# Performance work log

Measured on AMD Instinct MI355X. Metric: run time of the kernel, lower is better.

Reference implementation:

```python
import jax, jax.numpy as jnp
import numpy as np
import math

B, T, C = 8, 1024, 1024
H = 16
D = C // H
TI = 256
FF = 4 * C
EPS = 1e-5


def _ln(x, g, b):
    mu = jnp.mean(x, axis=-1, keepdims=True)
    var = jnp.mean(jnp.square(x - mu), axis=-1, keepdims=True)
    return (x - mu) * jax.lax.rsqrt(var + EPS) * g + b


def _gelu_tanh(x):
    return jax.nn.gelu(x, approximate=True)


def setup_inputs() -> dict:
    key = jax.random.key(0)
    ks = jax.random.split(key, 16)
    s = 0.02
    inp = {
        'x': jax.random.normal(ks[0], (B, T, C), jnp.float32),
        'x_img_feats': jax.random.normal(ks[1], (B, TI, C), jnp.float32),
        'ln1_g': jnp.ones((C,), jnp.float32), 'ln1_b': jnp.zeros((C,), jnp.float32),
        'ln2_g': jnp.ones((C,), jnp.float32), 'ln2_b': jnp.zeros((C,), jnp.float32),
        'W_attn': jax.random.normal(ks[2], (C, 3 * C), jnp.float32) * s,
        'b_attn': jnp.zeros((3 * C,), jnp.float32),
        'W_aproj': jax.random.normal(ks[3], (C, C), jnp.float32) * s,
        'b_aproj': jnp.zeros((C,), jnp.float32),
        'Wq': jax.random.normal(ks[4], (C, C), jnp.float32) * s,
        'bq': jnp.zeros((C,), jnp.float32),
        'Wk': jax.random.normal(ks[5], (C, C), jnp.float32) * s,
        'bk': jnp.zeros((C,), jnp.float32),
        'Wv': jax.random.normal(ks[6], (C, C), jnp.float32) * s,
        'bv': jnp.zeros((C,), jnp.float32),
        'Wcproj': jax.random.normal(ks[7], (C, C), jnp.float32) * s,
        'bcproj': jnp.zeros((C,), jnp.float32),
        'W_fc': jax.random.normal(ks[8], (C, FF), jnp.float32) * s,
        'b_fc': jnp.zeros((FF,), jnp.float32),
        'W_mproj': jax.random.normal(ks[9], (FF, C), jnp.float32) * s,
        'b_mproj': jnp.zeros((C,), jnp.float32),
    }
    return inp


def _heads(t):
    # (B, S, C) -> (B, H, S, D)
    return t.reshape(t.shape[0], t.shape[1], H, D).transpose(0, 2, 1, 3)


def _merge(t):
    # (B, H, S, D) -> (B, S, C)
    return t.transpose(0, 2, 1, 3).reshape(t.shape[0], t.shape[2], C)


def reference(x, x_img_feats, ln1_g, ln1_b, ln2_g, ln2_b,
              W_attn, b_attn, W_aproj, b_aproj,
              Wq, bq, Wk, bk, Wv, bv, Wcproj, bcproj,
              W_fc, b_fc, W_mproj, b_mproj):
    scale = 1.0 / math.sqrt(D)

    # causal self-attention
    h = _ln(x, ln1_g, ln1_b)
    qkv = h @ W_attn + b_attn
    q, k, v = jnp.split(qkv, 3, axis=-1)
    q, k, v = _heads(q), _heads(k), _heads(v)
    att = jnp.einsum('bhtd,bhsd->bhts', q, k) * scale
    causal = jnp.tril(jnp.ones((T, T), bool))
    att = jnp.where(causal[None, None], att, -jnp.inf)
    att = jax.nn.softmax(att, axis=-1)
    sa = _merge(jnp.einsum('bhts,bhsd->bhtd', att, v)) @ W_aproj + b_aproj
    x = x + sa

    # cross-attention (text queries, image keys/values)
    ht = _ln(x, ln1_g, ln1_b)
    q = _heads(ht @ Wq + bq)
    k = _heads(x_img_feats @ Wk + bk)
    v = _heads(x_img_feats @ Wv + bv)
    catt = jax.nn.softmax(jnp.einsum('bhtd,bhsd->bhts', q, k) * scale, axis=-1)
    ca = _merge(jnp.einsum('bhts,bhsd->bhtd', catt, v)) @ Wcproj + bcproj
    x = x + ca

    # MLP
    h2 = _ln(x, ln2_g, ln2_b)
    x = x + _gelu_tanh(h2 @ W_fc + b_fc) @ W_mproj + b_mproj
    return x
```

## Files before the change

### kernel.cpp

```cpp
#include <hip/hip_runtime.h>

#define B_ 8
#define T_ 1024
#define C_ 1024
#define H_ 16
#define D_ 64
#define TI_ 256
#define FF_ 4096
#define BT_ (B_*T_)
#define BTI_ (B_*TI_)

typedef __bf16 bf16x8 __attribute__((ext_vector_type(8)));
typedef float f32x4 __attribute__((ext_vector_type(4)));
typedef float f32x16 __attribute__((ext_vector_type(16)));

__device__ __forceinline__ unsigned short f2bf(float f){
  unsigned u = __float_as_uint(f);
  u += 0x7fffu + ((u>>16)&1u);
  return (unsigned short)(u>>16);
}

__device__ __forceinline__ void cp16(const void* g, void* l){
  __builtin_amdgcn_global_load_lds(
      (const __attribute__((address_space(1))) unsigned int*)(unsigned long long)g,
      (__attribute__((address_space(3))) unsigned int*)(unsigned long long)l,
      16, 0, 0);
}

template<int MODE>
__global__ __launch_bounds__(256, 3) void gemm_bt(
    const unsigned short* __restrict__ A,
    const unsigned short* __restrict__ Bt,
    const float* __restrict__ bias,
    const float* __restrict__ resid,
    void* __restrict__ outp,
    int M, int N, int K, int nkind, int tshift)
{
  __shared__ unsigned short sA[128*64];
  __shared__ unsigned short sB[128*64];
  const int tid  = threadIdx.x;
  const int wid  = tid >> 6;
  const int lane = tid & 63;
  const int l32  = lane & 31;
  const int khalf = lane >> 5;

  const int row0 = blockIdx.y * 128;
  const int col0 = blockIdx.x * 128;
  const int wr = (wid >> 1) * 64;
  const int wc = (wid & 1) * 64;

  const unsigned short* gp[8];
  unsigned short* lp[8];
#pragma unroll
  for (int r=0;r<8;r++){
    int chunk = wid*8 + r;
    int cA = chunk & 15;
    int slot = cA*64 + lane;
    int row = slot >> 3;
    int cc = (slot & 7) ^ (row & 7);
    if (chunk < 16){
      gp[r] = A  + (size_t)(row0+row)*K + cc*8;
      lp[r] = sA + cA*512;
    } else {
      gp[r] = Bt + (size_t)(col0+row)*K + cc*8;
      lp[r] = sB + cA*512;
    }
  }

  f32x16 acc[2][2];
#pragma unroll
  for (int i=0;i<2;i++)
#pragma unroll
    for (int j=0;j<2;j++)
#pragma unroll
      for (int r=0;r<16;r++) acc[i][j][r] = 0.f;

  for (int k0 = 0; k0 < K; k0 += 64){
    if (k0) __syncthreads();
#pragma unroll
    for (int r=0;r<8;r++)
      cp16(gp[r] + k0, lp[r]);
    __syncthreads();
    const char* sAb = (const char*)sA;
    const char* sBb = (const char*)sB;
#pragma unroll
    for (int kk=0;kk<4;kk++){
      bf16x8 af[2], bfb[2];
#pragma unroll
      for (int i=0;i<2;i++){
        int rr = wr + i*32 + l32;
        af[i] = *(const bf16x8*)(sAb + rr*128 + ((((kk<<1)+khalf) ^ (rr&7))<<4));
      }
#pragma unroll
      for (int j=0;j<2;j++){
        int rr = wc + j*32 + l32;
        bfb[j] = *(const bf16x8*)(sBb + rr*128 + ((((kk<<1)+khalf) ^ (rr&7))<<4));
      }
#pragma unroll
      for (int i=0;i<2;i++)
#pragma unroll
        for (int j=0;j<2;j++)
          acc[i][j] = __builtin_amdgcn_mfma_f32_32x32x16_bf16(af[i], bfb[j], acc[i][j], 0, 0, 0);
    }
  }

#pragma unroll
  for (int j=0;j<2;j++){
    int gc = col0 + wc + j*32 + l32;
    float bz = bias[gc];
#pragma unroll
    for (int i=0;i<2;i++){
      int gr_base = row0 + wr + i*32 + 4*khalf;
#pragma unroll
      for (int reg=0; reg<16; ++reg){
        int gr = gr_base + (reg&3) + 8*(reg>>2);
        float v = acc[i][j][reg] + bz;
        if (MODE == 1){
          float w = 1.5957691216057308f*(v + 0.044715f*v*v*v);
          float g = v / (1.f + __expf(-w));
          ((unsigned short*)outp)[(size_t)gr*N + gc] = f2bf(g);
        } else if (MODE == 2){
          size_t idx = (size_t)gr*N + gc;
          ((float*)outp)[idx] = resid[idx] + v;
        } else {
          int kind = gc >> 10;
          int hc = gc & 1023;
          int hh = hc >> 6;
          int d  = hc & 63;
          int bb = gr >> tshift;
          int tt = gr & ((1<<tshift)-1);
          size_t oidx = ((((size_t)(bb*16 + hh)*nkind + kind) << tshift) + tt)*64 + d;
          ((unsigned short*)outp)[oidx] = f2bf(v);
        }
      }
    }
  }
}

__global__ __launch_bounds__(256) void ln_fwd(
    const float* __restrict__ x, const float* __restrict__ g,
    const float* __restrict__ b, unsigned short* __restrict__ out)
{
  int row = blockIdx.x, t = threadIdx.x;
  const float4* xv = (const float4*)(x + (size_t)row*C_);
  float4 v = xv[t];
  float s  = v.x+v.y+v.z+v.w;
  float ss = v.x*v.x + v.y*v.y + v.z*v.z + v.w*v.w;
#pragma unroll
  for (int o=32;o>0;o>>=1){ s += __shfl_down(s,o); ss += __shfl_down(ss,o); }
  __shared__ float red[16];
  int wid = t>>6, lane = t&63;
  if (lane==0){ red[wid]=s; red[8+wid]=ss; }
  __syncthreads();
  if (t==0){
    red[0] = red[0]+red[1]+red[2]+red[3];
    red[8] = red[8]+red[9]+red[10]+red[11];
  }
  __syncthreads();
  float mu  = red[0] * (1.f/C_);
  float var = red[8] * (1.f/C_) - mu*mu;
  float rstd = rsqrtf(var + 1e-5f);
  float4 gv = ((const float4*)g)[t];
  float4 bv = ((const float4*)b)[t];
  ushort4 o;
  o.x = f2bf((v.x-mu)*rstd*gv.x + bv.x);
  o.y = f2bf((v.y-mu)*rstd*gv.y + bv.y);
  o.z = f2bf((v.z-mu)*rstd*gv.z + bv.z);
  o.w = f2bf((v.w-mu)*rstd*gv.w + bv.w);
  ((ushort4*)(out + (size_t)row*C_))[t] = o;
}

__global__ void wconv_t(const float* __restrict__ W, unsigned short* __restrict__ Wt,
                        int Kd, int Nd)
{
  __shared__ float tile[32][33];
  int tx = threadIdx.x, ty = threadIdx.y;
  int n0 = blockIdx.x*32, k0 = blockIdx.y*32;
#pragma unroll
  for (int j=0;j<4;j++)
    tile[ty+8*j][tx] = W[(size_t)(k0+ty+8*j)*Nd + (n0+tx)];
  __syncthreads();
#pragma unroll
  for (int j=0;j<4;j++)
    Wt[(size_t)(n0+ty+8*j)*Kd + (k0+tx)] = f2bf(tile[tx][ty+8*j]);
}

__global__ void wconv_t5(const float* W0, const float* W1, const float* W2,
                         const float* W3, const float* W4,
                         unsigned short* O0, unsigned short* O1, unsigned short* O2,
                         unsigned short* O3, unsigned short* O4)
{
  __shared__ float tile[32][33];
  const float* Ws[5] = {W0,W1,W2,W3,W4};
  unsigned short* Os[5] = {O0,O1,O2,O3,O4};
  const float* W = Ws[blockIdx.z];
  unsigned short* Wt = Os[blockIdx.z];
  int tx = threadIdx.x, ty = threadIdx.y;
  int n0 = blockIdx.x*32, k0 = blockIdx.y*32;
#pragma unroll
  for (int j=0;j<4;j++)
    tile[ty+8*j][tx] = W[(size_t)(k0+ty+8*j)*1024 + (n0+tx)];
  __syncthreads();
#pragma unroll
  for (int j=0;j<4;j++)
    Wt[(size_t)(n0+ty+8*j)*1024 + (k0+tx)] = f2bf(tile[tx][ty+8*j]);
}

#define PREP_N1 (BT_*C_/4)
#define PREP_N2 (BTI_*C_/4)
__global__ void prep_misc(const float* __restrict__ x, float* __restrict__ xcur,
                          const float* __restrict__ ximg, unsigned short* __restrict__ ximg_bf,
                          const float* __restrict__ bk, const float* __restrict__ bv,
                          float* __restrict__ bkv)
{
  int i = blockIdx.x*256 + threadIdx.x;
  if (i < PREP_N1){
    ((float4*)xcur)[i] = ((const float4*)x)[i];
  } else if (i < PREP_N1 + PREP_N2){
    int k = i - PREP_N1;
    float4 v = ((const float4*)ximg)[k];
    ushort4 o; o.x=f2bf(v.x); o.y=f2bf(v.y); o.z=f2bf(v.z); o.w=f2bf(v.w);
    ((ushort4*)ximg_bf)[k] = o;
  } else if (i < PREP_N1 + PREP_N2 + 512){
    int k = i - PREP_N1 - PREP_N2;
    ((float4*)bkv)[k] = (k < 256) ? ((const float4*)bk)[k] : ((const float4*)bv)[k-256];
  }
}

__global__ __launch_bounds__(256) void attn_fwd(
    const unsigned short* __restrict__ Qb, unsigned int sQ,
    const unsigned short* __restrict__ Kb, const unsigned short* __restrict__ Vb,
    unsigned int sKV, int causal, int nkb_in,
    unsigned short* __restrict__ Out, float scale)
{
  __shared__ unsigned short sK[64*64];
  __shared__ unsigned short sV[64*64];
  __shared__ unsigned short sP[4*16*64];
  const int tid = threadIdx.x;
  const int wid = tid >> 6;
  const int lane = tid & 63;
  const int quad = lane >> 4;
  const int l16 = lane & 15;

  const int L = blockIdx.x;
  const int g  = (L & 7) + (L >> 7) * 8;
  const int qt = 15 - ((L >> 3) & 15);
  const int b = g >> 4, h = g & 15;
  const float c2 = scale * 1.4426950408889634f;

  const unsigned short* Qp = Qb + (size_t)g * sQ;
  const unsigned short* Kp = Kb + (size_t)g * sKV;
  const unsigned short* Vp = Vb + (size_t)g * sKV;

  const int qrow = qt*64 + wid*16 + l16;
  const unsigned short* qb = Qp + (size_t)qrow*64;
  bf16x8 qf[2];
  qf[0] = *(const bf16x8*)(qb + quad*8);
  qf[1] = *(const bf16x8*)(qb + 32 + quad*8);

  f32x4 zero = {0.f,0.f,0.f,0.f};
  f32x4 O[4];
#pragma unroll
  for (int j=0;j<4;j++) O[j] = zero;
  float mrun[4], lrun[4];
#pragma unroll
  for (int r=0;r<4;r++){ mrun[r] = -1e30f; lrun[r] = 0.f; }

  const int nkb = causal ? (qt+1) : nkb_in;
  char* sPw = (char*)sP + wid*2048;

  for (int kb=0; kb<nkb; ++kb){
    if (kb) __syncthreads();
#pragma unroll
    for (int ss=0; ss<2; ++ss){
      int slot = tid + ss*256;
      int srow = slot >> 3;
      int cc = (slot & 7) ^ (srow & 7);
      cp16(Kp + (size_t)kb*4096 + srow*64 + cc*8, sK + (size_t)(wid*64 + ss*256)*8);
    }
    {
      int s_ = lane;
      int dbase = wid*16;
      const unsigned short* gv = Vp + (size_t)kb*4096 + s_*64 + dbase;
      unsigned short vals[16];
      *(uint4*)(vals)   = *(const uint4*)(gv);
      *(uint4*)(vals+8) = *(const uint4*)(gv+8);
      int chunk = s_ >> 3;
      int sb = (s_ & 7)*2;
#pragma unroll
      for (int jj=0; jj<16; ++jj){
        int d = dbase + jj;
        *(unsigned short*)((char*)sV + d*128 + ((chunk ^ (d&7))<<4) + sb) = vals[jj];
      }
    }
    __syncthreads();

    f32x4 sacc[4];
#pragma unroll
    for (int j=0;j<4;j++) sacc[j] = zero;
#pragma unroll
    for (int j=0;j<4;j++){
      int krow = j*16 + l16;
#pragma unroll
      for (int kk=0;kk<2;kk++){
        bf16x8 kf = *(const bf16x8*)((const char*)sK + krow*128 + (((kk*4+quad) ^ (krow&7))<<4));
        sacc[j] = __builtin_amdgcn_mfma_f32_16x16x32_bf16(qf[kk], kf, sacc[j], 0, 0, 0);
      }
    }
    const int qa0 = qt*64 + wid*16 + quad*4;
    float sc[4][4];
#pragma unroll
    for (int j=0;j<4;j++){
      int key = kb*64 + j*16 + l16;
#pragma unroll
      for (int r=0;r<4;r++){
        float v = sacc[j][r];
        if (causal && key > qa0 + r) v = -1e30f;
        sc[j][r] = v;
      }
    }
    float mnew[4], alpha[4], rs[4];
#pragma unroll
    for (int r=0;r<4;r++){
      float m = fmaxf(fmaxf(sc[0][r], sc[1][r]), fmaxf(sc[2][r], sc[3][r]));
#pragma unroll
      for (int msk=1; msk<16; msk<<=1) m = fmaxf(m, __shfl_xor(m, msk));
      mnew[r] = fmaxf(mrun[r], m);
      alpha[r] = exp2f((mrun[r] - mnew[r]) * c2);
      mrun[r] = mnew[r];
      rs[r] = 0.f;
    }
#pragma unroll
    for (int j=0;j<4;j++){
#pragma unroll
      for (int r=0;r<4;r++){
        float p = exp2f((sc[j][r] - mnew[r]) * c2);
        rs[r] += p;
        int prow = quad*4 + r;
        int cole = j*16 + l16;
        *(unsigned short*)(sPw + prow*128 + (((cole>>3) ^ (prow&7))<<4) + (cole&7)*2) = f2bf(p);
      }
    }
#pragma unroll
    for (int r=0;r<4;r++){
#pragma unroll
      for (int msk=1; msk<16; msk<<=1) rs[r] += __shfl_xor(rs[r], msk);
      lrun[r] = lrun[r]*alpha[r] + rs[r];
    }
#pragma unroll
    for (int j=0;j<4;j++){
      O[j][0] *= alpha[0]; O[j][1] *= alpha[1];
      O[j][2] *= alpha[2]; O[j][3] *= alpha[3];
    }
    bf16x8 pf[2];
#pragma unroll
    for (int kk=0;kk<2;kk++)
      pf[kk] = *(const bf16x8*)(sPw + l16*128 + (((kk*4+quad) ^ (l16&7))<<4));
#pragma unroll
    for (int j=0;j<4;j++){
      int vrow = j*16 + l16;
#pragma unroll
      for (int kk=0;kk<2;kk++){
        bf16x8 vf = *(const bf16x8*)((const char*)sV + vrow*128 + (((kk*4+quad) ^ (vrow&7))<<4));
        O[j] = __builtin_amdgcn_mfma_f32_16x16x32_bf16(pf[kk], vf, O[j], 0, 0, 0);
      }
    }
  }
#pragma unroll
  for (int j=0;j<4;j++){
#pragma unroll
    for (int r=0;r<4;r++){
      int qa = qt*64 + wid*16 + quad*4 + r;
      float o = O[j][r] / lrun[r];
      Out[(size_t)(b*T_ + qa)*C_ + h*64 + j*16 + l16] = f2bf(o);
    }
  }
}

extern "C" void kernel_launch(void* const* d_in, const int* in_sizes, int n_in,
                              void* d_out, int out_size, void* d_ws, size_t ws_size,
                              hipStream_t stream)
{
  const float* x       = (const float*)d_in[0];
  const float* ximg    = (const float*)d_in[1];
  const float* ln1_g   = (const float*)d_in[2];
  const float* ln1_b   = (const float*)d_in[3];
  const float* ln2_g   = (const float*)d_in[4];
  const float* ln2_b   = (const float*)d_in[5];
  const float* W_attn  = (const float*)d_in[6];
  const float* b_attn  = (const float*)d_in[7];
  const float* W_aproj = (const float*)d_in[8];
  const float* b_aproj = (const float*)d_in[9];
  const float* Wq = (const float*)d_in[10];
  const float* bq = (const float*)d_in[11];
  const float* Wk = (const float*)d_in[12];
  const float* bk = (const float*)d_in[13];
  const float* Wv = (const float*)d_in[14];
  const float* bv = (const float*)d_in[15];
  const float* Wcproj  = (const float*)d_in[16];
  const float* bcproj  = (const float*)d_in[17];
  const float* W_fc    = (const float*)d_in[18];
  const float* b_fc    = (const float*)d_in[19];
  const float* W_mproj = (const float*)d_in[20];
  const float* b_mproj = (const float*)d_in[21];

  char* ws = (char*)d_ws;
  unsigned short* wt_attn  = (unsigned short*)(ws + 0);
  unsigned short* wt_aproj = (unsigned short*)(ws + 6291456);
  unsigned short* wt_q     = (unsigned short*)(ws + 8388608);
  unsigned short* wt_k     = (unsigned short*)(ws + 10485760);
  unsigned short* wt_v     = (unsigned short*)(ws + 12582912);
  unsigned short* wt_cproj = (unsigned short*)(ws + 14680064);
  unsigned short* wt_fc    = (unsigned short*)(ws + 16777216);
  unsigned short* wt_mproj = (unsigned short*)(ws + 25165824);
  unsigned short* ximg_bf  = (unsigned short*)(ws + 33554432);
  float*          xcur     = (float*)(ws + 37748736);
  unsigned short* h_bf     = (unsigned short*)(ws + 71303168);
  unsigned short* qkv_hm   = (unsigned short*)(ws + 88080384);
  unsigned short* att_out  = (unsigned short*)(ws + 88080384 + 50331648);
  unsigned short* u_bf     = (unsigned short*)(ws + 88080384);
  unsigned short* q2_hm    = (unsigned short*)(ws + 155189248);
  unsigned short* kv2_hm   = (unsigned short*)(ws + 171966464);
  unsigned short* ca       = (unsigned short*)(ws + 180355072);
  float*          bkv      = (float*)(ws + 197132288);

  dim3 tb(32,8);
  wconv_t5<<<dim3(32,32,5), tb, 0, stream>>>(W_aproj, Wq, Wk, Wv, Wcproj,
                                             wt_aproj, wt_q, wt_k, wt_v, wt_cproj);
  wconv_t<<<dim3(96,32),  tb, 0, stream>>>(W_attn,  wt_attn,  1024, 3072);
  wconv_t<<<dim3(128,32), tb, 0, stream>>>(W_fc,    wt_fc,    1024, 4096);
  wconv_t<<<dim3(32,128), tb, 0, stream>>>(W_mproj, wt_mproj, 4096, 1024);
  prep_misc<<<(PREP_N1+PREP_N2+512+255)/256, 256, 0, stream>>>(
      x, xcur, ximg, ximg_bf, bk, bv, bkv);

  ln_fwd<<<BT_, 256, 0, stream>>>(x, ln1_g, ln1_b, h_bf);
  gemm_bt<3><<<dim3(24,64), 256, 0, stream>>>(h_bf, wt_attn, b_attn, nullptr, qkv_hm,
                                              BT_, 3072, 1024, 3, 10);
  attn_fwd<<<2048, 256, 0, stream>>>(qkv_hm, 3*T_*D_, qkv_hm + T_*D_, qkv_hm + 2*T_*D_,
                                     3*T_*D_, 1, 16, att_out, 0.125f);
  gemm_bt<2><<<dim3(8,64), 256, 0, stream>>>(att_out, wt_aproj, b_aproj, xcur, xcur,
                                             BT_, 1024, 1024, 0, 0);

  ln_fwd<<<BT_, 256, 0, stream>>>(xcur, ln1_g, ln1_b, h_bf);
  gemm_bt<3><<<dim3(8,64), 256, 0, stream>>>(h_bf, wt_q, bq, nullptr, q2_hm,
                                             BT_, 1024, 1024, 1, 10);
  gemm_bt<3><<<dim3(16,16), 256, 0, stream>>>(ximg_bf, wt_k, bkv, nullptr, kv2_hm,
                                              BTI_, 2048, 1024, 2, 8);
  attn_fwd<<<2048, 256, 0, stream>>>(q2_hm, T_*D_, kv2_hm, kv2_hm + TI_*D_,
                                     2*TI_*D_, 0, 4, ca, 0.125f);
  gemm_bt<2><<<dim3(8,64), 256, 0, stream>>>(ca, wt_cproj, bcproj, xcur, xcur,
                                             BT_, 1024, 1024, 0, 0);

  ln_fwd<<<BT_, 256, 0, stream>>>(xcur, ln2_g, ln2_b, h_bf);
  gemm_bt<1><<<dim3(32,64), 256, 0, stream>>>(h_bf, wt_fc, b_fc, nullptr, u_bf,
                                              BT_, 4096, 1024, 0, 0);
  gemm_bt<2><<<dim3(8,64), 256, 0, stream>>>(u_bf, wt_mproj, b_mproj, xcur, (float*)d_out,
                                             BT_, 1024, 4096, 0, 0);
}
```

Measured before the change: 722.2 us.

## Process two query tiles per attention block to reuse K/V loads

Each attention block now handles 128 query rows as two 64-row sub-tiles that share each K/V tile staged in LDS, which halves the grid size and the K/V global traffic per query. Causal masking is applied only on diagonal tiles, and fully masked sub-tiles are skipped. The softmax row sum now comes from an MFMA of P against a ones vector instead of shuffle reductions, and P is converted to bf16 by truncation rather than rounding. Costs: more registers per thread, fewer blocks to fill the GPU, and slightly different numerics in P and the row sum.

```diff
diff --git a/kernel.cpp b/kernel.cpp
--- a/kernel.cpp
+++ b/kernel.cpp
@@ -18,6 +18,9 @@
   unsigned u = __float_as_uint(f);
   u += 0x7fffu + ((u>>16)&1u);
   return (unsigned short)(u>>16);
+}
+__device__ __forceinline__ unsigned short f2bf_t(float f){
+  return (unsigned short)(__float_as_uint(f)>>16);
 }
 
 __device__ __forceinline__ void cp16(const void* g, void* l){
@@ -243,8 +246,9 @@
   const int l16 = lane & 15;
 
   const int L = blockIdx.x;
-  const int g  = (L & 7) + (L >> 7) * 8;
-  const int qt = 15 - ((L >> 3) & 15);
+  const int g  = (L & 7) + (L >> 6) * 8;
+  int qt = (L >> 3) & 7;
+  if (causal) qt = 7 - qt;
   const int b = g >> 4, h = g & 15;
   const float c2 = scale * 1.4426950408889634f;
 
@@ -252,21 +256,32 @@
   const unsigned short* Kp = Kb + (size_t)g * sKV;
   const unsigned short* Vp = Vb + (size_t)g * sKV;
 
-  const int qrow = qt*64 + wid*16 + l16;
-  const unsigned short* qb = Qp + (size_t)qrow*64;
-  bf16x8 qf[2];
-  qf[0] = *(const bf16x8*)(qb + quad*8);
-  qf[1] = *(const bf16x8*)(qb + 32 + quad*8);
+  bf16x8 qf[2][2];
+#pragma unroll
+  for (int s=0;s<2;s++){
+    int qrow = qt*128 + s*64 + wid*16 + l16;
+    const unsigned short* qb = Qp + (size_t)qrow*64;
+    qf[s][0] = *(const bf16x8*)(qb + quad*8);
+    qf[s][1] = *(const bf16x8*)(qb + 32 + quad*8);
+  }
+
+  bf16x8 ones;
+#pragma unroll
+  for (int k=0;k<8;k++) ones[k] = (__bf16)1.0f;
 
   f32x4 zero = {0.f,0.f,0.f,0.f};
-  f32x4 O[4];
-#pragma unroll
-  for (int j=0;j<4;j++) O[j] = zero;
-  float mrun[4], lrun[4];
-#pragma unroll
-  for (int r=0;r<4;r++){ mrun[r] = -1e30f; lrun[r] = 0.f; }
-
-  const int nkb = causal ? (qt+1) : nkb_in;
+  f32x4 O[2][4];
+#pragma unroll
+  for (int s=0;s<2;s++)
+#pragma unroll
+    for (int j=0;j<4;j++) O[s][j] = zero;
+  float mrun[2][4], lrun[2][4];
+#pragma unroll
+  for (int s=0;s<2;s++)
+#pragma unroll
+    for (int r=0;r<4;r++){ mrun[s][r] = -1e30f; lrun[s][r] = 0.f; }
+
+  const int nkb = causal ? (2*qt + 2) : nkb_in;
   char* sPw = (char*)sP + wid*2048;
 
   for (int kb=0; kb<nkb; ++kb){
@@ -295,84 +310,97 @@
     }
     __syncthreads();
 
-    f32x4 sacc[4];
-#pragma unroll
-    for (int j=0;j<4;j++) sacc[j] = zero;
+#pragma unroll
+    for (int s=0; s<2; ++s){
+      const int qb0 = qt*128 + s*64;
+      if (causal && kb*64 > qb0 + 63) continue;
+      const bool need_mask = causal && (kb*64 + 63 > qb0);
+
+      f32x4 sacc[4];
+#pragma unroll
+      for (int j=0;j<4;j++) sacc[j] = zero;
+#pragma unroll
+      for (int j=0;j<4;j++){
+        int krow = j*16 + l16;
+#pragma unroll
+        for (int kk=0;kk<2;kk++){
+          bf16x8 kf = *(const bf16x8*)((const char*)sK + krow*128 + (((kk*4+quad) ^ (krow&7))<<4));
+          sacc[j] = __builtin_amdgcn_mfma_f32_16x16x32_bf16(qf[s][kk], kf, sacc[j], 0, 0, 0);
+        }
+      }
+      const int qa0 = qb0 + wid*16 + quad*4;
+      float sc[4][4];
+      if (need_mask){
+#pragma unroll
+        for (int j=0;j<4;j++){
+          int key = kb*64 + j*16 + l16;
+#pragma unroll
+          for (int r=0;r<4;r++)
+            sc[j][r] = (key > qa0 + r) ? -1e30f : sacc[j][r];
+        }
+      } else {
+#pragma unroll
+        for (int j=0;j<4;j++)
+#pragma unroll
+          for (int r=0;r<4;r++) sc[j][r] = sacc[j][r];
+      }
+      float mnew[4], alpha[4];
+#pragma unroll
+      for (int r=0;r<4;r++){
+        float m = fmaxf(fmaxf(sc[0][r], sc[1][r]), fmaxf(sc[2][r], sc[3][r]));
+#pragma unroll
+        for (int msk=1; msk<16; msk<<=1) m = fmaxf(m, __shfl_xor(m, msk));
+        mnew[r] = fmaxf(mrun[s][r], m);
+        alpha[r] = exp2f((mrun[s][r] - mnew[r]) * c2);
+        mrun[s][r] = mnew[r];
+      }
+#pragma unroll
+      for (int j=0;j<4;j++){
+#pragma unroll
+        for (int r=0;r<4;r++){
+          float p = exp2f((sc[j][r] - mnew[r]) * c2);
+          int prow = quad*4 + r;
+          int cole = j*16 + l16;
+          *(unsigned short*)(sPw + prow*128 + (((cole>>3) ^ (prow&7))<<4) + (cole&7)*2) = f2bf_t(p);
+        }
+      }
+      bf16x8 pf[2];
+#pragma unroll
+      for (int kk=0;kk<2;kk++)
+        pf[kk] = *(const bf16x8*)(sPw + l16*128 + (((kk*4+quad) ^ (l16&7))<<4));
+      f32x4 racc = zero;
+      racc = __builtin_amdgcn_mfma_f32_16x16x32_bf16(pf[0], ones, racc, 0, 0, 0);
+      racc = __builtin_amdgcn_mfma_f32_16x16x32_bf16(pf[1], ones, racc, 0, 0, 0);
+#pragma unroll
+      for (int r=0;r<4;r++)
+        lrun[s][r] = lrun[s][r]*alpha[r] + racc[r];
+#pragma unroll
+      for (int j=0;j<4;j++){
+        O[s][j][0] *= alpha[0]; O[s][j][1] *= alpha[1];
+        O[s][j][2] *= alpha[2]; O[s][j][3] *= alpha[3];
+      }
+#pragma unroll
+      for (int j=0;j<4;j++){
+        int vrow = j*16 + l16;
+#pragma unroll
+        for (int kk=0;kk<2;kk++){
+          bf16x8 vf = *(const bf16x8*)((const char*)sV + vrow*128 + (((kk*4+quad) ^ (vrow&7))<<4));
+          O[s][j] = __builtin_amdgcn_mfma_f32_16x16x32_bf16(pf[kk], vf, O[s][j], 0, 0, 0);
+        }
+      }
+    }
+  }
+
+#pragma unroll
+  for (int s=0;s<2;s++){
 #pragma unroll
     for (int j=0;j<4;j++){
-      int krow = j*16 + l16;
-#pragma unroll
-      for (int kk=0;kk<2;kk++){
-        bf16x8 kf = *(const bf16x8*)((const char*)sK + krow*128 + (((kk*4+quad) ^ (krow&7))<<4));
-        sacc[j] = __builtin_amdgcn_mfma_f32_16x16x32_bf16(qf[kk], kf, sacc[j], 0, 0, 0);
-      }
-    }
-    const int qa0 = qt*64 + wid*16 + quad*4;
-    float sc[4][4];
-#pragma unroll
-    for (int j=0;j<4;j++){
-      int key = kb*64 + j*16 + l16;
 #pragma unroll
       for (int r=0;r<4;r++){
-        float v = sacc[j][r];
-        if (causal && key > qa0 + r) v = -1e30f;
-        sc[j][r] = v;
-      }
-    }
-    float mnew[4], alpha[4], rs[4];
-#pragma unroll
-    for (int r=0;r<4;r++){
-      float m = fmaxf(fmaxf(sc[0][r], sc[1][r]), fmaxf(sc[2][r], sc[3][r]));
-#pragma unroll
-      for (int msk=1; msk<16; msk<<=1) m = fmaxf(m, __shfl_xor(m, msk));
-      mnew[r] = fmaxf(mrun[r], m);
-      alpha[r] = exp2f((mrun[r] - mnew[r]) * c2);
-      mrun[r] = mnew[r];
-      rs[r] = 0.f;
-    }
-#pragma unroll
-    for (int j=0;j<4;j++){
-#pragma unroll
-      for (int r=0;r<4;r++){
-        float p = exp2f((sc[j][r] - mnew[r]) * c2);
-        rs[r] += p;
-        int prow = quad*4 + r;
-        int cole = j*16 + l16;
-        *(unsigned short*)(sPw + prow*128 + (((cole>>3) ^ (prow&7))<<4) + (cole&7)*2) = f2bf(p);
-      }
-    }
-#pragma unroll
-    for (int r=0;r<4;r++){
-#pragma unroll
-      for (int msk=1; msk<16; msk<<=1) rs[r] += __shfl_xor(rs[r], msk);
-      lrun[r] = lrun[r]*alpha[r] + rs[r];
-    }
-#pragma unroll
-    for (int j=0;j<4;j++){
-      O[j][0] *= alpha[0]; O[j][1] *= alpha[1];
-      O[j][2] *= alpha[2]; O[j][3] *= alpha[3];
-    }
-    bf16x8 pf[2];
-#pragma unroll
-    for (int kk=0;kk<2;kk++)
-      pf[kk] = *(const bf16x8*)(sPw + l16*128 + (((kk*4+quad) ^ (l16&7))<<4));
-#pragma unroll
-    for (int j=0;j<4;j++){
-      int vrow = j*16 + l16;
-#pragma unroll
-      for (int kk=0;kk<2;kk++){
-        bf16x8 vf = *(const bf16x8*)((const char*)sV + vrow*128 + (((kk*4+quad) ^ (vrow&7))<<4));
-        O[j] = __builtin_amdgcn_mfma_f32_16x16x32_bf16(pf[kk], vf, O[j], 0, 0, 0);
-      }
-    }
-  }
-#pragma unroll
-  for (int j=0;j<4;j++){
-#pragma unroll
-    for (int r=0;r<4;r++){
-      int qa = qt*64 + wid*16 + quad*4 + r;
-      float o = O[j][r] / lrun[r];
-      Out[(size_t)(b*T_ + qa)*C_ + h*64 + j*16 + l16] = f2bf(o);
+        int qa = qt*128 + s*64 + wid*16 + quad*4 + r;
+        float o = O[s][j][r] / lrun[s][r];
+        Out[(size_t)(b*T_ + qa)*C_ + h*64 + j*16 + l16] = f2bf(o);
+      }
     }
   }
 }
@@ -436,7 +464,7 @@
   ln_fwd<<<BT_, 256, 0, stream>>>(x, ln1_g, ln1_b, h_bf);
   gemm_bt<3><<<dim3(24,64), 256, 0, stream>>>(h_bf, wt_attn, b_attn, nullptr, qkv_hm,
                                               BT_, 3072, 1024, 3, 10);
-  attn_fwd<<<2048, 256, 0, stream>>>(qkv_hm, 3*T_*D_, qkv_hm + T_*D_, qkv_hm + 2*T_*D_,
+  attn_fwd<<<1024, 256, 0, stream>>>(qkv_hm, 3*T_*D_, qkv_hm + T_*D_, qkv_hm + 2*T_*D_,
                                      3*T_*D_, 1, 16, att_out, 0.125f);
   gemm_bt<2><<<dim3(8,64), 256, 0, stream>>>(att_out, wt_aproj, b_aproj, xcur, xcur,
                                              BT_, 1024, 1024, 0, 0);
@@ -446,7 +474,7 @@
                                              BT_, 1024, 1024, 1, 10);
   gemm_bt<3><<<dim3(16,16), 256, 0, stream>>>(ximg_bf, wt_k, bkv, nullptr, kv2_hm,
                                               BTI_, 2048, 1024, 2, 8);
-  attn_fwd<<<2048, 256, 0, stream>>>(q2_hm, T_*D_, kv2_hm, kv2_hm + TI_*D_,
+  attn_fwd<<<1024, 256, 0, stream>>>(q2_hm, T_*D_, kv2_hm, kv2_hm + TI_*D_,
                                      2*TI_*D_, 0, 4, ca, 0.125f);
   gemm_bt<2><<<dim3(8,64), 256, 0, stream>>>(ca, wt_cproj, bcproj, xcur, xcur,
                                              BT_, 1024, 1024, 0, 0);
```

New measurement: 725.2 us. About the same (+0.4%).
